# Optimization experiments

Measured on AMD Instinct MI355X. Metric: run time of the kernel, lower is better.

## Reference

```python
import jax, jax.numpy as jnp
import numpy as np

# dims
B, C, H, W = 2, 256, 128, 256
P, G = 9, 8            # num_pts, num_groups
GC = C // G            # group_channels


def setup_inputs() -> dict:
    key = jax.random.key(0)
    ks = jax.random.split(key, 8)
    s = 0.02
    return {
        "feats1": jax.random.normal(ks[0], (B, C, H, W), jnp.float32),
        "feats2": jax.random.normal(ks[1], (B, C, H, W), jnp.float32),
        "anchor_points": jax.random.uniform(ks[2], (B, H * W, 2), jnp.float32),
        "norm1_g": jnp.ones((C,), jnp.float32), "norm1_b": jnp.zeros((C,), jnp.float32),
        "norm2_g": jnp.ones((C,), jnp.float32), "norm2_b": jnp.zeros((C,), jnp.float32),
        "Wv": jax.random.normal(ks[3], (C, C), jnp.float32) * s, "bv": jnp.zeros((C,), jnp.float32),
        "Ww": jax.random.normal(ks[4], (C, G * P), jnp.float32) * s, "bw": jnp.zeros((G * P,), jnp.float32),
        "Wk": jax.random.normal(ks[5], (C, P), jnp.float32) * s, "bk": jnp.zeros((P,), jnp.float32),
        "Wo": jax.random.normal(ks[6], (C, C), jnp.float32) * s, "bo": jnp.zeros((C,), jnp.float32),
    }


def _ln(x, g, b):
    # LayerNorm over the last (channel) axis, eps as torch default
    m = jnp.mean(x, axis=-1, keepdims=True)
    v = jnp.mean(jnp.square(x - m), axis=-1, keepdims=True)
    return (x - m) * jax.lax.rsqrt(v + 1e-5) * g + b


def _bilinear_sample(value, pts):
    # value: (b, H, W, C); pts: (b, N, 2) normalized [0,1] (x, y)
    # grid_sample semantics: align_corners=False, zero padding
    b, h, w, c = value.shape
    x = pts[..., 0] * w - 0.5
    y = pts[..., 1] * h - 0.5
    x0 = jnp.floor(x)
    y0 = jnp.floor(y)
    wx = (x - x0)[..., None]
    wy = (y - y0)[..., None]
    x0i = x0.astype(jnp.int32)
    y0i = y0.astype(jnp.int32)
    vflat = value.reshape(b, h * w, c)

    def gather(yi, xi):
        valid = (yi >= 0) & (yi < h) & (xi >= 0) & (xi < w)
        idx = jnp.clip(yi, 0, h - 1) * w + jnp.clip(xi, 0, w - 1)
        g = jnp.take_along_axis(vflat, idx[..., None], axis=1)
        return g * valid[..., None].astype(value.dtype)

    v00 = gather(y0i, x0i)
    v01 = gather(y0i, x0i + 1)
    v10 = gather(y0i + 1, x0i)
    v11 = gather(y0i + 1, x0i + 1)
    return (v00 * (1 - wx) * (1 - wy) + v01 * wx * (1 - wy)
            + v10 * (1 - wx) * wy + v11 * wx * wy)


def reference(feats1, feats2, anchor_points, norm1_g, norm1_b, norm2_g, norm2_b,
              Wv, bv, Ww, bw, Wk, bk, Wo, bo):
    b, c, h, w = feats1.shape
    hw = h * w
    # to_3d(dim=2): (b, c, h, w) -> (b, hw, c); LayerNorm over c
    x1 = _ln(feats1.reshape(b, c, hw).transpose(0, 2, 1), norm1_g, norm1_b)
    x2 = _ln(feats2.reshape(b, c, hw).transpose(0, 2, 1), norm2_g, norm2_b)

    # value_proj (1x1 conv == per-pixel linear)
    value = (x2 @ Wv + bv).reshape(b, h, w, c)

    # weight_proj -> (b, hw, P, G); channel layout p*G + g; softmax over the P points per group
    logits = (x1 @ Ww + bw).reshape(b, hw, P, G)
    wts = jax.nn.softmax(logits, axis=2)

    # 1D key-point generator: per-pixel learned offsets along x around the anchor
    off = x1 @ Wk + bk                                   # (b, hw, P) normalized offsets
    kx = anchor_points[..., 0:1] + off                   # (b, hw, P)
    ky = jnp.broadcast_to(anchor_points[..., 1:2], kx.shape)
    kp = jnp.stack([kx, ky], axis=-1)                    # (b, hw, P, 2)

    # deformable aggregation: bilinear gather + group-weighted sum over points
    samp = _bilinear_sample(value, kp.reshape(b, hw * P, 2)).reshape(b, hw, P, G, GC)
    agg = jnp.einsum('bnpgc,bnpg->bngc', samp, wts).reshape(b, hw, c)

    out = (agg @ Wo + bo).reshape(b, h, w, c).transpose(0, 3, 1, 2)  # (b, c, h, w)
    return out, kp.reshape(b, h, w, P, 2)
```

## Files before the change

### kernel.cpp

```cpp
#include <hip/hip_runtime.h>
#include <hip/hip_bf16.h>


constexpr int B = 2, C = 256, H = 128, W = 256;
constexpr int HW = H * W;
constexpr int P = 9, G = 8;
constexpr int PIX = 32;
constexpr int NPIX = B * HW;

typedef __attribute__((ext_vector_type(8))) __bf16 bf16x8;
typedef __attribute__((ext_vector_type(4))) float f32x4;

static __device__ __forceinline__ unsigned short f2bf(float x) {
    __hip_bfloat16 h = __float2bfloat16(x);
    return *reinterpret_cast<unsigned short*>(&h);
}
static __device__ __forceinline__ unsigned int pack2(float a, float b) {
    return (unsigned int)f2bf(a) | ((unsigned int)f2bf(b) << 16);
}
static __device__ __forceinline__ bf16x8 ldb8(const unsigned short* p) {
    return *reinterpret_cast<const bf16x8*>(p);
}

__global__ __launch_bounds__(256) void k_prep(
    const float* __restrict__ Ww, const float* __restrict__ Wv,
    const float* __restrict__ Wo,
    unsigned short* __restrict__ WwT, unsigned short* __restrict__ WvT,
    unsigned short* __restrict__ WoT)
{
    int tid = blockIdx.x * 256 + threadIdx.x;
    if (tid < 20480) {
        int n = tid >> 8, k = tid & 255;
        float v = (n < 72) ? Ww[k * 72 + n] : 0.f;
        WwT[tid] = f2bf(v);
    } else if (tid < 20480 + 65536) {
        int i = tid - 20480;
        int n = i >> 8, k = i & 255;
        WvT[i] = f2bf(Wv[k * 256 + n]);
    } else {
        int i = tid - 86016;
        int n = i >> 8, k = i & 255;
        WoT[i] = f2bf(Wo[k * 256 + n]);
    }
}

__global__ __launch_bounds__(256) void k1_ln1(
    const float* __restrict__ feats1,
    const float* __restrict__ anchor,
    const float* __restrict__ g1, const float* __restrict__ b1,
    const float* __restrict__ Wk, const float* __restrict__ bk,
    unsigned short* __restrict__ x1b, float* __restrict__ kp_out)
{
    __shared__ float X[PIX][C + 1];
    __shared__ float red[2][8][PIX];
    __shared__ float meanA[PIX], rstdA[PIX];

    const int t = threadIdx.x;
    const int p = t & 31;
    const int part = t >> 5;
    const int gpix0 = blockIdx.x * PIX;
    const int b = gpix0 >> 15;
    const int n0 = gpix0 & (HW - 1);
    const float* Fb = feats1 + (size_t)b * C * HW;

    #pragma unroll
    for (int i = 0; i < 32; ++i) {
        int c = i * 8 + part;
        X[p][c] = Fb[(size_t)c * HW + n0 + p];
    }
    __syncthreads();

    float s = 0.f, ss = 0.f;
    #pragma unroll
    for (int i = 0; i < 32; ++i) {
        float v = X[p][part * 32 + i];
        s += v; ss += v * v;
    }
    red[0][part][p] = s; red[1][part][p] = ss;
    __syncthreads();
    if (part == 0) {
        float s2 = 0.f, ss2 = 0.f;
        #pragma unroll
        for (int k = 0; k < 8; ++k) { s2 += red[0][k][p]; ss2 += red[1][k][p]; }
        float mean = s2 * (1.f / C);
        float var  = ss2 * (1.f / C) - mean * mean;
        meanA[p] = mean; rstdA[p] = rsqrtf(var + 1e-5f);
    }
    __syncthreads();
    {
        float mean = meanA[p], rstd = rstdA[p];
        #pragma unroll
        for (int i = 0; i < 32; ++i) {
            int c = part * 32 + i;
            X[p][c] = (X[p][c] - mean) * rstd * g1[c] + b1[c];
        }
    }
    __syncthreads();

    {
        unsigned short* row = x1b + ((size_t)gpix0 + p) * C + part * 32;
        #pragma unroll
        for (int i4 = 0; i4 < 8; ++i4) {
            uint2 u;
            u.x = pack2(X[p][part * 32 + i4 * 4 + 0], X[p][part * 32 + i4 * 4 + 1]);
            u.y = pack2(X[p][part * 32 + i4 * 4 + 2], X[p][part * 32 + i4 * 4 + 3]);
            *reinterpret_cast<uint2*>(row + i4 * 4) = u;
        }
    }

    const size_t pixg = (size_t)gpix0 + p;
    const float ax = anchor[pixg * 2 + 0];
    const float ay = anchor[pixg * 2 + 1];
    for (int j = 72 + part; j < 81; j += 8) {
        int pt = j - 72;
        float acc = bk[pt];
        #pragma unroll 4
        for (int c = 0; c < C; ++c) acc += X[p][c] * Wk[c * P + pt];
        size_t o = (pixg * P + pt) * 2;
        kp_out[o] = ax + acc;
        kp_out[o + 1] = ay;
    }
}

__global__ __launch_bounds__(256) void k2_ln2(
    const float* __restrict__ feats2,
    const float* __restrict__ g2, const float* __restrict__ b2,
    unsigned short* __restrict__ x2b)
{
    __shared__ float X[PIX][C + 1];
    __shared__ float red[2][8][PIX];
    __shared__ float meanA[PIX], rstdA[PIX];

    const int t = threadIdx.x;
    const int p = t & 31;
    const int part = t >> 5;
    const int gpix0 = blockIdx.x * PIX;
    const int b = gpix0 >> 15;
    const int n0 = gpix0 & (HW - 1);
    const float* Fb = feats2 + (size_t)b * C * HW;

    #pragma unroll
    for (int i = 0; i < 32; ++i) {
        int c = i * 8 + part;
        X[p][c] = Fb[(size_t)c * HW + n0 + p];
    }
    __syncthreads();

    float s = 0.f, ss = 0.f;
    #pragma unroll
    for (int i = 0; i < 32; ++i) {
        float v = X[p][part * 32 + i];
        s += v; ss += v * v;
    }
    red[0][part][p] = s; red[1][part][p] = ss;
    __syncthreads();
    if (part == 0) {
        float s2 = 0.f, ss2 = 0.f;
        #pragma unroll
        for (int k = 0; k < 8; ++k) { s2 += red[0][k][p]; ss2 += red[1][k][p]; }
        float mean = s2 * (1.f / C);
        float var  = ss2 * (1.f / C) - mean * mean;
        meanA[p] = mean; rstdA[p] = rsqrtf(var + 1e-5f);
    }
    __syncthreads();
    {
        float mean = meanA[p], rstd = rstdA[p];
        unsigned short* row = x2b + ((size_t)gpix0 + p) * C + part * 32;
        #pragma unroll
        for (int i4 = 0; i4 < 8; ++i4) {
            float v0 = (X[p][part * 32 + i4 * 4 + 0] - mean) * rstd * g2[part * 32 + i4 * 4 + 0] + b2[part * 32 + i4 * 4 + 0];
            float v1 = (X[p][part * 32 + i4 * 4 + 1] - mean) * rstd * g2[part * 32 + i4 * 4 + 1] + b2[part * 32 + i4 * 4 + 1];
            float v2 = (X[p][part * 32 + i4 * 4 + 2] - mean) * rstd * g2[part * 32 + i4 * 4 + 2] + b2[part * 32 + i4 * 4 + 2];
            float v3 = (X[p][part * 32 + i4 * 4 + 3] - mean) * rstd * g2[part * 32 + i4 * 4 + 3] + b2[part * 32 + i4 * 4 + 3];
            uint2 u; u.x = pack2(v0, v1); u.y = pack2(v2, v3);
            *reinterpret_cast<uint2*>(row + i4 * 4) = u;
        }
    }
}

__global__ __launch_bounds__(256) void k_gemmw(
    const unsigned short* __restrict__ x1b,
    const unsigned short* __restrict__ WwT,
    const float* __restrict__ bw,
    float* __restrict__ wts)
{
    __shared__ float L[128][81];

    const int t = threadIdx.x;
    const int wave = t >> 6, lane = t & 63;
    const int m_base = blockIdx.x * 128;
    const int m0 = m_base + wave * 32;
    const int l15 = lane & 15, quad = lane >> 4;

    f32x4 acc[2][5];
    #pragma unroll
    for (int ms = 0; ms < 2; ++ms)
        #pragma unroll
        for (int ns = 0; ns < 5; ++ns)
            acc[ms][ns] = (f32x4){0.f, 0.f, 0.f, 0.f};

    size_t aoff[2], boff[5];
    #pragma unroll
    for (int ms = 0; ms < 2; ++ms)
        aoff[ms] = (size_t)(m0 + ms * 16 + l15) * 256 + quad * 8;
    #pragma unroll
    for (int ns = 0; ns < 5; ++ns)
        boff[ns] = (size_t)(ns * 16 + l15) * 256 + quad * 8;

    for (int kk = 0; kk < 8; ++kk) {
        bf16x8 a[2], bfr[5];
        #pragma unroll
        for (int ms = 0; ms < 2; ++ms) a[ms] = ldb8(x1b + aoff[ms] + kk * 32);
        #pragma unroll
        for (int ns = 0; ns < 5; ++ns) bfr[ns] = ldb8(WwT + boff[ns] + kk * 32);
        #pragma unroll
        for (int ms = 0; ms < 2; ++ms)
            #pragma unroll
            for (int ns = 0; ns < 5; ++ns)
                acc[ms][ns] = __builtin_amdgcn_mfma_f32_16x16x32_bf16(a[ms], bfr[ns], acc[ms][ns], 0, 0, 0);
    }

    float bias[5];
    #pragma unroll
    for (int ns = 0; ns < 5; ++ns) {
        int n = ns * 16 + l15;
        bias[ns] = (n < 72) ? bw[n] : 0.f;
    }
    #pragma unroll
    for (int ms = 0; ms < 2; ++ms) {
        #pragma unroll
        for (int ns = 0; ns < 5; ++ns) {
            int n = ns * 16 + l15;
            if (n < 72) {
                #pragma unroll
                for (int r = 0; r < 4; ++r) {
                    int ml = wave * 32 + ms * 16 + quad * 4 + r;
                    L[ml][n] = acc[ms][ns][r] + bias[ns];
                }
            }
        }
    }
    __syncthreads();

    for (int tau = t; tau < 1024; tau += 256) {
        int px = tau >> 3, g = tau & 7;
        float m = -1e30f;
        #pragma unroll
        for (int pt = 0; pt < P; ++pt) m = fmaxf(m, L[px][pt * 8 + g]);
        float e[P], sum = 0.f;
        #pragma unroll
        for (int pt = 0; pt < P; ++pt) { e[pt] = __expf(L[px][pt * 8 + g] - m); sum += e[pt]; }
        float inv = 1.f / sum;
        float* wb = wts + (size_t)(m_base + px) * 72 + g * 9;
        #pragma unroll
        for (int pt = 0; pt < P; ++pt) wb[pt] = e[pt] * inv;
    }
}

__global__ __launch_bounds__(256) void k_gemmv(
    const unsigned short* __restrict__ x2b,
    const unsigned short* __restrict__ WvT,
    const float* __restrict__ bv,
    unsigned short* __restrict__ val)
{
    const int t = threadIdx.x;
    const int wave = t >> 6, lane = t & 63;
    const int m_base = blockIdx.x * 64;
    const int n0 = wave * 64;
    const int l15 = lane & 15, quad = lane >> 4;

    f32x4 acc[4][4];
    #pragma unroll
    for (int ms = 0; ms < 4; ++ms)
        #pragma unroll
        for (int ns = 0; ns < 4; ++ns)
            acc[ms][ns] = (f32x4){0.f, 0.f, 0.f, 0.f};

    size_t aoff[4], boff[4];
    #pragma unroll
    for (int ms = 0; ms < 4; ++ms)
        aoff[ms] = (size_t)(m_base + ms * 16 + l15) * 256 + quad * 8;
    #pragma unroll
    for (int ns = 0; ns < 4; ++ns)
        boff[ns] = (size_t)(n0 + ns * 16 + l15) * 256 + quad * 8;

    for (int kk = 0; kk < 8; ++kk) {
        bf16x8 a[4], bfr[4];
        #pragma unroll
        for (int ms = 0; ms < 4; ++ms) a[ms] = ldb8(x2b + aoff[ms] + kk * 32);
        #pragma unroll
        for (int ns = 0; ns < 4; ++ns) bfr[ns] = ldb8(WvT + boff[ns] + kk * 32);
        #pragma unroll
        for (int ms = 0; ms < 4; ++ms)
            #pragma unroll
            for (int ns = 0; ns < 4; ++ns)
                acc[ms][ns] = __builtin_amdgcn_mfma_f32_16x16x32_bf16(a[ms], bfr[ns], acc[ms][ns], 0, 0, 0);
    }

    float bvr[4];
    #pragma unroll
    for (int ns = 0; ns < 4; ++ns) bvr[ns] = bv[n0 + ns * 16 + l15];

    #pragma unroll
    for (int ms = 0; ms < 4; ++ms) {
        #pragma unroll
        for (int ns = 0; ns < 4; ++ns) {
            int n = n0 + ns * 16 + l15;
            #pragma unroll
            for (int r = 0; r < 4; ++r) {
                int pix = m_base + ms * 16 + quad * 4 + r;
                val[(size_t)pix * 256 + n] = f2bf(acc[ms][ns][r] + bvr[ns]);
            }
        }
    }
}

__global__ __launch_bounds__(256) void k_gather(
    const float* __restrict__ wts,
    const float* __restrict__ kp,
    const unsigned short* __restrict__ val,
    unsigned short* __restrict__ aggb)
{
    __shared__ float Wl[PIX][72];
    __shared__ float KPl[PIX][18];

    const int t = threadIdx.x;
    const int gpix0 = blockIdx.x * PIX;
    const int b = gpix0 >> 15;

    for (int f = t; f < PIX * 72; f += 256)
        ((float*)Wl)[f] = wts[(size_t)gpix0 * 72 + f];
    for (int f = t; f < PIX * 18; f += 256)
        ((float*)KPl)[f] = kp[(size_t)gpix0 * 18 + f];
    __syncthreads();

    const int wave = t >> 6, lane = t & 63;
    const int gl = lane >> 3;
    const unsigned short* vbp = val + (size_t)b * HW * 256 + 4 * lane;

    for (int px = wave; px < PIX; px += 4) {
        const float ay = KPl[px][1];
        float yf = ay * (float)H - 0.5f;
        float y0f = floorf(yf);
        float wy = yf - y0f;
        int y0 = (int)y0f;
        float vy0 = ((unsigned)y0 < (unsigned)H) ? 1.f : 0.f;
        float vy1 = ((unsigned)(y0 + 1) < (unsigned)H) ? 1.f : 0.f;
        int y0c = min(max(y0, 0), H - 1);
        int y1c = min(max(y0 + 1, 0), H - 1);

        float a0 = 0.f, a1 = 0.f, a2 = 0.f, a3 = 0.f;

        #pragma unroll
        for (int pt = 0; pt < P; ++pt) {
            float kx = KPl[px][2 * pt];
            float w  = Wl[px][gl * 9 + pt];
            float xf = kx * (float)W - 0.5f;
            float x0f = floorf(xf);
            float wx = xf - x0f;
            int x0 = (int)x0f;
            float vx0 = ((unsigned)x0 < (unsigned)W) ? 1.f : 0.f;
            float vx1 = ((unsigned)(x0 + 1) < (unsigned)W) ? 1.f : 0.f;
            int x0c = min(max(x0, 0), W - 1);
            int x1c = min(max(x0 + 1, 0), W - 1);

            float c00 = w * (1.f - wx) * (1.f - wy) * vy0 * vx0;
            float c01 = w * wx * (1.f - wy) * vy0 * vx1;
            float c10 = w * (1.f - wx) * wy * vy1 * vx0;
            float c11 = w * wx * wy * vy1 * vx1;

            uint2 u00 = *(const uint2*)(vbp + ((size_t)(y0c * W + x0c) << 8));
            uint2 u01 = *(const uint2*)(vbp + ((size_t)(y0c * W + x1c) << 8));
            uint2 u10 = *(const uint2*)(vbp + ((size_t)(y1c * W + x0c) << 8));
            uint2 u11 = *(const uint2*)(vbp + ((size_t)(y1c * W + x1c) << 8));

            a0 += c00 * __uint_as_float(u00.x << 16) + c01 * __uint_as_float(u01.x << 16)
                + c10 * __uint_as_float(u10.x << 16) + c11 * __uint_as_float(u11.x << 16);
            a1 += c00 * __uint_as_float(u00.x & 0xffff0000u) + c01 * __uint_as_float(u01.x & 0xffff0000u)
                + c10 * __uint_as_float(u10.x & 0xffff0000u) + c11 * __uint_as_float(u11.x & 0xffff0000u);
            a2 += c00 * __uint_as_float(u00.y << 16) + c01 * __uint_as_float(u01.y << 16)
                + c10 * __uint_as_float(u10.y << 16) + c11 * __uint_as_float(u11.y << 16);
            a3 += c00 * __uint_as_float(u00.y & 0xffff0000u) + c01 * __uint_as_float(u01.y & 0xffff0000u)
                + c10 * __uint_as_float(u10.y & 0xffff0000u) + c11 * __uint_as_float(u11.y & 0xffff0000u);
        }

        uint2 o;
        o.x = pack2(a0, a1);
        o.y = pack2(a2, a3);
        *reinterpret_cast<uint2*>(aggb + ((size_t)(gpix0 + px) << 8) + 4 * lane) = o;
    }
}

__global__ __launch_bounds__(256) void k_gemmo(
    const unsigned short* __restrict__ aggb,
    const unsigned short* __restrict__ WoT,
    const float* __restrict__ bo,
    float* __restrict__ out)
{
    const int t = threadIdx.x;
    const int wave = t >> 6, lane = t & 63;
    const int n_base = blockIdx.x * 64;
    const int b = n_base >> 15;
    const int hw0 = n_base & (HW - 1);
    const int m0 = wave * 64;
    const int l15 = lane & 15, quad = lane >> 4;

    f32x4 acc[4][4];
    #pragma unroll
    for (int ms = 0; ms < 4; ++ms)
        #pragma unroll
        for (int ns = 0; ns < 4; ++ns)
            acc[ms][ns] = (f32x4){0.f, 0.f, 0.f, 0.f};

    size_t aoff[4], boff[4];
    #pragma unroll
    for (int ms = 0; ms < 4; ++ms)
        aoff[ms] = (size_t)(m0 + ms * 16 + l15) * 256 + quad * 8;
    #pragma unroll
    for (int ns = 0; ns < 4; ++ns)
        boff[ns] = (size_t)(n_base + ns * 16 + l15) * 256 + quad * 8;

    for (int kk = 0; kk < 8; ++kk) {
        bf16x8 a[4], bfr[4];
        #pragma unroll
        for (int ms = 0; ms < 4; ++ms) a[ms] = ldb8(WoT + aoff[ms] + kk * 32);
        #pragma unroll
        for (int ns = 0; ns < 4; ++ns) bfr[ns] = ldb8(aggb + boff[ns] + kk * 32);
        #pragma unroll
        for (int ms = 0; ms < 4; ++ms)
            #pragma unroll
            for (int ns = 0; ns < 4; ++ns)
                acc[ms][ns] = __builtin_amdgcn_mfma_f32_16x16x32_bf16(a[ms], bfr[ns], acc[ms][ns], 0, 0, 0);
    }

    float bor[4][4];
    #pragma unroll
    for (int ms = 0; ms < 4; ++ms)
        #pragma unroll
        for (int r = 0; r < 4; ++r)
            bor[ms][r] = bo[m0 + ms * 16 + quad * 4 + r];

    #pragma unroll
    for (int ms = 0; ms < 4; ++ms) {
        #pragma unroll
        for (int ns = 0; ns < 4; ++ns) {
            #pragma unroll
            for (int r = 0; r < 4; ++r) {
                int ch = m0 + ms * 16 + quad * 4 + r;
                int pixn = ns * 16 + l15;
                out[((size_t)b * 256 + ch) * HW + hw0 + pixn] = acc[ms][ns][r] + bor[ms][r];
            }
        }
    }
}

extern "C" void kernel_launch(void* const* d_in, const int* in_sizes, int n_in,
                              void* d_out, int out_size, void* d_ws, size_t ws_size,
                              hipStream_t stream)
{
    const float* feats1 = (const float*)d_in[0];
    const float* feats2 = (const float*)d_in[1];
    const float* anchor = (const float*)d_in[2];
    const float* n1g    = (const float*)d_in[3];
    const float* n1b    = (const float*)d_in[4];
    const float* n2g    = (const float*)d_in[5];
    const float* n2b    = (const float*)d_in[6];
    const float* Wv     = (const float*)d_in[7];
    const float* bv     = (const float*)d_in[8];
    const float* Ww     = (const float*)d_in[9];
    const float* bw     = (const float*)d_in[10];
    const float* Wk     = (const float*)d_in[11];
    const float* bk     = (const float*)d_in[12];
    const float* Wo     = (const float*)d_in[13];
    const float* bo     = (const float*)d_in[14];

    float* out = (float*)d_out;
    float* kp  = out + (size_t)B * C * HW;

    unsigned short* R1  = (unsigned short*)d_ws;
    unsigned short* val = (unsigned short*)((char*)d_ws + 33554432);
    float*          wts = (float*)((char*)d_ws + 67108864);
    unsigned short* WwT = (unsigned short*)((char*)d_ws + 85983232);
    unsigned short* WvT = WwT + 20480;
    unsigned short* WoT = WvT + 65536;

    k_prep <<<592,  256, 0, stream>>>(Ww, Wv, Wo, WwT, WvT, WoT);
    k1_ln1 <<<2048, 256, 0, stream>>>(feats1, anchor, n1g, n1b, Wk, bk, R1, kp);
    k_gemmw<<<512,  256, 0, stream>>>(R1, WwT, bw, wts);
    k2_ln2 <<<2048, 256, 0, stream>>>(feats2, n2g, n2b, R1);
    k_gemmv<<<1024, 256, 0, stream>>>(R1, WvT, bv, val);
    k_gather<<<2048,256, 0, stream>>>(wts, kp, val, R1);
    k_gemmo<<<1024, 256, 0, stream>>>(R1, WoT, bo, out);
}
```

Before: 457.4 us.

## Fuse LayerNorms with projection GEMMs and reorder gather by anchor row buckets

```diff
diff --git a/kernel.cpp b/kernel.cpp
--- a/kernel.cpp
+++ b/kernel.cpp
@@ -7,6 +7,7 @@
 constexpr int P = 9, G = 8;
 constexpr int PIX = 32;
 constexpr int NPIX = B * HW;
+constexpr int NBKT = 2 * 129;
 
 typedef __attribute__((ext_vector_type(8))) __bf16 bf16x8;
 typedef __attribute__((ext_vector_type(4))) float f32x4;
@@ -18,7 +19,10 @@
 static __device__ __forceinline__ unsigned int pack2(float a, float b) {
     return (unsigned int)f2bf(a) | ((unsigned int)f2bf(b) << 16);
 }
-static __device__ __forceinline__ bf16x8 ldb8(const unsigned short* p) {
+static __device__ __forceinline__ float bf2f(unsigned short u) {
+    return __uint_as_float((unsigned int)u << 16);
+}
+static __device__ __forceinline__ bf16x8 ldb8g(const unsigned short* p) {
     return *reinterpret_cast<const bf16x8*>(p);
 }
 
@@ -31,8 +35,7 @@
     int tid = blockIdx.x * 256 + threadIdx.x;
     if (tid < 20480) {
         int n = tid >> 8, k = tid & 255;
-        float v = (n < 72) ? Ww[k * 72 + n] : 0.f;
-        WwT[tid] = f2bf(v);
+        WwT[tid] = f2bf((n < 72) ? Ww[k * 72 + n] : 0.f);
     } else if (tid < 20480 + 65536) {
         int i = tid - 20480;
         int n = i >> 8, k = i & 255;
@@ -44,16 +47,57 @@
     }
 }
 
-__global__ __launch_bounds__(256) void k1_ln1(
-    const float* __restrict__ feats1,
-    const float* __restrict__ anchor,
+static __device__ __forceinline__ int bucket_of(const float* anchor, int pix) {
+    float ay = anchor[(size_t)pix * 2 + 1];
+    int y0 = (int)floorf(ay * (float)H - 0.5f);
+    y0 = min(max(y0, -1), H - 1);
+    return (pix >> 15) * 129 + y0 + 1;
+}
+
+__global__ __launch_bounds__(256) void k_hist(
+    const float* __restrict__ anchor, int* __restrict__ hist)
+{
+    int pix = blockIdx.x * 256 + threadIdx.x;
+    atomicAdd(&hist[bucket_of(anchor, pix)], 1);
+}
+
+__global__ __launch_bounds__(256) void k_scan(
+    const int* __restrict__ hist, int* __restrict__ cursor)
+{
+    __shared__ int h[NBKT];
+    int t = threadIdx.x;
+    for (int i = t; i < NBKT; i += 256) h[i] = hist[i];
+    __syncthreads();
+    if (t == 0) {
+        int run = 0;
+        for (int i = 0; i < NBKT; ++i) { int v = h[i]; cursor[i] = run; run += v; }
+    }
+}
+
+__global__ __launch_bounds__(256) void k_scatter(
+    const float* __restrict__ anchor, int* __restrict__ cursor,
+    int* __restrict__ perm)
+{
+    int pix = blockIdx.x * 256 + threadIdx.x;
+    int pos = atomicAdd(&cursor[bucket_of(anchor, pix)], 1);
+    perm[pos] = pix;
+}
+
+__global__ __launch_bounds__(256) void kA(
+    const float* __restrict__ feats1, const float* __restrict__ anchor,
     const float* __restrict__ g1, const float* __restrict__ b1,
     const float* __restrict__ Wk, const float* __restrict__ bk,
-    unsigned short* __restrict__ x1b, float* __restrict__ kp_out)
-{
-    __shared__ float X[PIX][C + 1];
-    __shared__ float red[2][8][PIX];
-    __shared__ float meanA[PIX], rstdA[PIX];
+    const unsigned short* __restrict__ WwT, const float* __restrict__ bw,
+    unsigned short* __restrict__ wtsb, float* __restrict__ kp_out)
+{
+    __shared__ unsigned short Hi[PIX][264];
+    __shared__ __align__(16) char smB[20480];
+    __shared__ float meanA[PIX], rstdA[PIX], axL[PIX], ayL[PIX];
+
+    float* WkL  = (float*)smB;
+    float* red2 = (float*)(smB + 9216);
+    float* red  = (float*)(smB + 18432);
+    float* Lg   = (float*)smB;
 
     const int t = threadIdx.x;
     const int p = t & 31;
@@ -63,71 +107,132 @@
     const int n0 = gpix0 & (HW - 1);
     const float* Fb = feats1 + (size_t)b * C * HW;
 
-    #pragma unroll
-    for (int i = 0; i < 32; ++i) {
-        int c = i * 8 + part;
-        X[p][c] = Fb[(size_t)c * HW + n0 + p];
-    }
-    __syncthreads();
+    for (int i = t; i < 2304; i += 256) WkL[i] = Wk[i];
+    if (t < PIX) {
+        axL[t] = anchor[((size_t)gpix0 + t) * 2 + 0];
+        ayL[t] = anchor[((size_t)gpix0 + t) * 2 + 1];
+    }
+
+    float x[32];
+    #pragma unroll
+    for (int i = 0; i < 32; ++i)
+        x[i] = Fb[(size_t)(part * 32 + i) * HW + n0 + p];
 
     float s = 0.f, ss = 0.f;
     #pragma unroll
-    for (int i = 0; i < 32; ++i) {
-        float v = X[p][part * 32 + i];
-        s += v; ss += v * v;
-    }
-    red[0][part][p] = s; red[1][part][p] = ss;
+    for (int i = 0; i < 32; ++i) { s += x[i]; ss += x[i] * x[i]; }
+    red[part * 32 + p] = s;
+    red[256 + part * 32 + p] = ss;
     __syncthreads();
     if (part == 0) {
         float s2 = 0.f, ss2 = 0.f;
         #pragma unroll
-        for (int k = 0; k < 8; ++k) { s2 += red[0][k][p]; ss2 += red[1][k][p]; }
+        for (int k = 0; k < 8; ++k) { s2 += red[k * 32 + p]; ss2 += red[256 + k * 32 + p]; }
         float mean = s2 * (1.f / C);
         float var  = ss2 * (1.f / C) - mean * mean;
         meanA[p] = mean; rstdA[p] = rsqrtf(var + 1e-5f);
     }
     __syncthreads();
+
     {
         float mean = meanA[p], rstd = rstdA[p];
         #pragma unroll
         for (int i = 0; i < 32; ++i) {
             int c = part * 32 + i;
-            X[p][c] = (X[p][c] - mean) * rstd * g1[c] + b1[c];
-        }
-    }
-    __syncthreads();
+            x[i] = (x[i] - mean) * rstd * g1[c] + b1[c];
+        }
+    }
 
     {
-        unsigned short* row = x1b + ((size_t)gpix0 + p) * C + part * 32;
-        #pragma unroll
-        for (int i4 = 0; i4 < 8; ++i4) {
-            uint2 u;
-            u.x = pack2(X[p][part * 32 + i4 * 4 + 0], X[p][part * 32 + i4 * 4 + 1]);
-            u.y = pack2(X[p][part * 32 + i4 * 4 + 2], X[p][part * 32 + i4 * 4 + 3]);
-            *reinterpret_cast<uint2*>(row + i4 * 4) = u;
-        }
-    }
-
-    const size_t pixg = (size_t)gpix0 + p;
-    const float ax = anchor[pixg * 2 + 0];
-    const float ay = anchor[pixg * 2 + 1];
-    for (int j = 72 + part; j < 81; j += 8) {
-        int pt = j - 72;
-        float acc = bk[pt];
+        float po[9];
+        #pragma unroll
+        for (int pt = 0; pt < 9; ++pt) po[pt] = 0.f;
         #pragma unroll 4
-        for (int c = 0; c < C; ++c) acc += X[p][c] * Wk[c * P + pt];
-        size_t o = (pixg * P + pt) * 2;
-        kp_out[o] = ax + acc;
-        kp_out[o + 1] = ay;
-    }
-}
-
-__global__ __launch_bounds__(256) void k2_ln2(
+        for (int i = 0; i < 32; ++i) {
+            int c = part * 32 + i;
+            float xv = x[i];
+            #pragma unroll
+            for (int pt = 0; pt < 9; ++pt) po[pt] += xv * WkL[c * 9 + pt];
+        }
+        #pragma unroll
+        for (int pt = 0; pt < 9; ++pt) red2[(part * 32 + p) * 9 + pt] = po[pt];
+    }
+
+    {
+        unsigned int* row = (unsigned int*)&Hi[p][part * 32];
+        #pragma unroll
+        for (int i = 0; i < 16; ++i) row[i] = pack2(x[2 * i], x[2 * i + 1]);
+    }
+    __syncthreads();
+
+    for (int tau = t; tau < 288; tau += 256) {
+        int px = tau & 31, pt = tau >> 5;
+        float off = bk[pt];
+        #pragma unroll
+        for (int k = 0; k < 8; ++k) off += red2[(k * 32 + px) * 9 + pt];
+        size_t o = (((size_t)gpix0 + px) * P + pt) * 2;
+        kp_out[o] = axL[px] + off;
+        kp_out[o + 1] = ayL[px];
+    }
+
+    const int wave = t >> 6, lane = t & 63;
+    const int l15 = lane & 15, quad = lane >> 4;
+    const int mt = wave & 1;
+    const int ntb = (wave >> 1) * 3;
+    const int ntc = (wave >> 1) ? 2 : 3;
+
+    f32x4 acc[3];
+    #pragma unroll
+    for (int j = 0; j < 3; ++j) acc[j] = (f32x4){0.f, 0.f, 0.f, 0.f};
+
+    const unsigned short* arow = &Hi[mt * 16 + l15][quad * 8];
+    for (int kk = 0; kk < 8; ++kk) {
+        bf16x8 a = *reinterpret_cast<const bf16x8*>(arow + kk * 32);
+        for (int j = 0; j < 3; ++j) {
+            if (j < ntc) {
+                bf16x8 bfr = ldb8g(WwT + (size_t)((ntb + j) * 16 + l15) * 256 + quad * 8 + kk * 32);
+                acc[j] = __builtin_amdgcn_mfma_f32_16x16x32_bf16(a, bfr, acc[j], 0, 0, 0);
+            }
+        }
+    }
+    __syncthreads();
+
+    #pragma unroll
+    for (int j = 0; j < 3; ++j) {
+        if (j < ntc) {
+            int n = (ntb + j) * 16 + l15;
+            if (n < 72) {
+                float bwn = bw[n];
+                #pragma unroll
+                for (int r = 0; r < 4; ++r)
+                    Lg[(mt * 16 + quad * 4 + r) * 81 + n] = acc[j][r] + bwn;
+            }
+        }
+    }
+    __syncthreads();
+
+    {
+        int px = t >> 3, g = t & 7;
+        float m = -1e30f;
+        #pragma unroll
+        for (int pt = 0; pt < P; ++pt) m = fmaxf(m, Lg[px * 81 + pt * 8 + g]);
+        float e[P], sum = 0.f;
+        #pragma unroll
+        for (int pt = 0; pt < P; ++pt) { e[pt] = __expf(Lg[px * 81 + pt * 8 + g] - m); sum += e[pt]; }
+        float inv = 1.f / sum;
+        unsigned short* wb = wtsb + ((size_t)gpix0 + px) * 72 + g * 9;
+        #pragma unroll
+        for (int pt = 0; pt < P; ++pt) wb[pt] = f2bf(e[pt] * inv);
+    }
+}
+
+__global__ __launch_bounds__(256) void kB(
     const float* __restrict__ feats2,
     const float* __restrict__ g2, const float* __restrict__ b2,
-    unsigned short* __restrict__ x2b)
-{
-    __shared__ float X[PIX][C + 1];
+    const unsigned short* __restrict__ WvT, const float* __restrict__ bv,
+    unsigned short* __restrict__ val)
+{
+    __shared__ unsigned short Hi[PIX][264];
     __shared__ float red[2][8][PIX];
     __shared__ float meanA[PIX], rstdA[PIX];
 
@@ -139,19 +244,14 @@
     const int n0 = gpix0 & (HW - 1);
     const float* Fb = feats2 + (size_t)b * C * HW;
 
-    #pragma unroll
-    for (int i = 0; i < 32; ++i) {
-        int c = i * 8 + part;
-        X[p][c] = Fb[(size_t)c * HW + n0 + p];
-    }
-    __syncthreads();
+    float x[32];
+    #pragma unroll
+    for (int i = 0; i < 32; ++i)
+        x[i] = Fb[(size_t)(part * 32 + i) * HW + n0 + p];
 
     float s = 0.f, ss = 0.f;
     #pragma unroll
-    for (int i = 0; i < 32; ++i) {
-        float v = X[p][part * 32 + i];
-        s += v; ss += v * v;
-    }
+    for (int i = 0; i < 32; ++i) { s += x[i]; ss += x[i] * x[i]; }
     red[0][part][p] = s; red[1][part][p] = ss;
     __syncthreads();
     if (part == 0) {
@@ -165,180 +265,92 @@
     __syncthreads();
     {
         float mean = meanA[p], rstd = rstdA[p];
-        unsigned short* row = x2b + ((size_t)gpix0 + p) * C + part * 32;
-        #pragma unroll
-        for (int i4 = 0; i4 < 8; ++i4) {
-            float v0 = (X[p][part * 32 + i4 * 4 + 0] - mean) * rstd * g2[part * 32 + i4 * 4 + 0] + b2[part * 32 + i4 * 4 + 0];
-            float v1 = (X[p][part * 32 + i4 * 4 + 1] - mean) * rstd * g2[part * 32 + i4 * 4 + 1] + b2[part * 32 + i4 * 4 + 1];
-            float v2 = (X[p][part * 32 + i4 * 4 + 2] - mean) * rstd * g2[part * 32 + i4 * 4 + 2] + b2[part * 32 + i4 * 4 + 2];
-            float v3 = (X[p][part * 32 + i4 * 4 + 3] - mean) * rstd * g2[part * 32 + i4 * 4 + 3] + b2[part * 32 + i4 * 4 + 3];
-            uint2 u; u.x = pack2(v0, v1); u.y = pack2(v2, v3);
-            *reinterpret_cast<uint2*>(row + i4 * 4) = u;
-        }
-    }
-}
-
-__global__ __launch_bounds__(256) void k_gemmw(
-    const unsigned short* __restrict__ x1b,
-    const unsigned short* __restrict__ WwT,
-    const float* __restrict__ bw,
-    float* __restrict__ wts)
-{
-    __shared__ float L[128][81];
-
-    const int t = threadIdx.x;
+        unsigned int* row = (unsigned int*)&Hi[p][part * 32];
+        #pragma unroll
+        for (int i = 0; i < 16; ++i) {
+            float v0 = (x[2 * i] - mean) * rstd * g2[part * 32 + 2 * i] + b2[part * 32 + 2 * i];
+            float v1 = (x[2 * i + 1] - mean) * rstd * g2[part * 32 + 2 * i + 1] + b2[part * 32 + 2 * i + 1];
+            row[i] = pack2(v0, v1);
+        }
+    }
+    __syncthreads();
+
     const int wave = t >> 6, lane = t & 63;
-    const int m_base = blockIdx.x * 128;
-    const int m0 = m_base + wave * 32;
     const int l15 = lane & 15, quad = lane >> 4;
-
-    f32x4 acc[2][5];
-    #pragma unroll
-    for (int ms = 0; ms < 2; ++ms)
-        #pragma unroll
-        for (int ns = 0; ns < 5; ++ns)
-            acc[ms][ns] = (f32x4){0.f, 0.f, 0.f, 0.f};
-
-    size_t aoff[2], boff[5];
-    #pragma unroll
-    for (int ms = 0; ms < 2; ++ms)
-        aoff[ms] = (size_t)(m0 + ms * 16 + l15) * 256 + quad * 8;
-    #pragma unroll
-    for (int ns = 0; ns < 5; ++ns)
-        boff[ns] = (size_t)(ns * 16 + l15) * 256 + quad * 8;
+    const int m0 = wave * 64;
+
+    f32x4 acc[4][2];
+    #pragma unroll
+    for (int ms = 0; ms < 4; ++ms)
+        #pragma unroll
+        for (int nt = 0; nt < 2; ++nt)
+            acc[ms][nt] = (f32x4){0.f, 0.f, 0.f, 0.f};
 
     for (int kk = 0; kk < 8; ++kk) {
-        bf16x8 a[2], bfr[5];
-        #pragma unroll
-        for (int ms = 0; ms < 2; ++ms) a[ms] = ldb8(x1b + aoff[ms] + kk * 32);
-        #pragma unroll
-        for (int ns = 0; ns < 5; ++ns) bfr[ns] = ldb8(WwT + boff[ns] + kk * 32);
-        #pragma unroll
-        for (int ms = 0; ms < 2; ++ms)
-            #pragma unroll
-            for (int ns = 0; ns < 5; ++ns)
-                acc[ms][ns] = __builtin_amdgcn_mfma_f32_16x16x32_bf16(a[ms], bfr[ns], acc[ms][ns], 0, 0, 0);
-    }
-
-    float bias[5];
-    #pragma unroll
-    for (int ns = 0; ns < 5; ++ns) {
-        int n = ns * 16 + l15;
-        bias[ns] = (n < 72) ? bw[n] : 0.f;
-    }
-    #pragma unroll
-    for (int ms = 0; ms < 2; ++ms) {
-        #pragma unroll
-        for (int ns = 0; ns < 5; ++ns) {
-            int n = ns * 16 + l15;
-            if (n < 72) {
-                #pragma unroll
-                for (int r = 0; r < 4; ++r) {
-                    int ml = wave * 32 + ms * 16 + quad * 4 + r;
-                    L[ml][n] = acc[ms][ns][r] + bias[ns];
-                }
-            }
-        }
-    }
-    __syncthreads();
-
-    for (int tau = t; tau < 1024; tau += 256) {
-        int px = tau >> 3, g = tau & 7;
-        float m = -1e30f;
-        #pragma unroll
-        for (int pt = 0; pt < P; ++pt) m = fmaxf(m, L[px][pt * 8 + g]);
-        float e[P], sum = 0.f;
-        #pragma unroll
-        for (int pt = 0; pt < P; ++pt) { e[pt] = __expf(L[px][pt * 8 + g] - m); sum += e[pt]; }
-        float inv = 1.f / sum;
-        float* wb = wts + (size_t)(m_base + px) * 72 + g * 9;
-        #pragma unroll
-        for (int pt = 0; pt < P; ++pt) wb[pt] = e[pt] * inv;
-    }
-}
-
-__global__ __launch_bounds__(256) void k_gemmv(
-    const unsigned short* __restrict__ x2b,
-    const unsigned short* __restrict__ WvT,
-    const float* __restrict__ bv,
-    unsigned short* __restrict__ val)
-{
-    const int t = threadIdx.x;
-    const int wave = t >> 6, lane = t & 63;
-    const int m_base = blockIdx.x * 64;
-    const int n0 = wave * 64;
-    const int l15 = lane & 15, quad = lane >> 4;
-
-    f32x4 acc[4][4];
-    #pragma unroll
-    for (int ms = 0; ms < 4; ++ms)
-        #pragma unroll
-        for (int ns = 0; ns < 4; ++ns)
-            acc[ms][ns] = (f32x4){0.f, 0.f, 0.f, 0.f};
-
-    size_t aoff[4], boff[4];
-    #pragma unroll
-    for (int ms = 0; ms < 4; ++ms)
-        aoff[ms] = (size_t)(m_base + ms * 16 + l15) * 256 + quad * 8;
-    #pragma unroll
-    for (int ns = 0; ns < 4; ++ns)
-        boff[ns] = (size_t)(n0 + ns * 16 + l15) * 256 + quad * 8;
-
-    for (int kk = 0; kk < 8; ++kk) {
-        bf16x8 a[4], bfr[4];
-        #pragma unroll
-        for (int ms = 0; ms < 4; ++ms) a[ms] = ldb8(x2b + aoff[ms] + kk * 32);
-        #pragma unroll
-        for (int ns = 0; ns < 4; ++ns) bfr[ns] = ldb8(WvT + boff[ns] + kk * 32);
+        bf16x8 a[4], bfr[2];
+        #pragma unroll
+        for (int ms = 0; ms < 4; ++ms)
+            a[ms] = ldb8g(WvT + (size_t)(m0 + ms * 16 + l15) * 256 + quad * 8 + kk * 32);
+        #pragma unroll
+        for (int nt = 0; nt < 2; ++nt)
+            bfr[nt] = *reinterpret_cast<const bf16x8*>(&Hi[nt * 16 + l15][quad * 8 + kk * 32]);
         #pragma unroll
         for (int ms = 0; ms < 4; ++ms)
             #pragma unroll
-            for (int ns = 0; ns < 4; ++ns)
-                acc[ms][ns] = __builtin_amdgcn_mfma_f32_16x16x32_bf16(a[ms], bfr[ns], acc[ms][ns], 0, 0, 0);
-    }
-
-    float bvr[4];
-    #pragma unroll
-    for (int ns = 0; ns < 4; ++ns) bvr[ns] = bv[n0 + ns * 16 + l15];
+            for (int nt = 0; nt < 2; ++nt)
+                acc[ms][nt] = __builtin_amdgcn_mfma_f32_16x16x32_bf16(a[ms], bfr[nt], acc[ms][nt], 0, 0, 0);
+    }
 
     #pragma unroll
     for (int ms = 0; ms < 4; ++ms) {
-        #pragma unroll
-        for (int ns = 0; ns < 4; ++ns) {
-            int n = n0 + ns * 16 + l15;
-            #pragma unroll
-            for (int r = 0; r < 4; ++r) {
-                int pix = m_base + ms * 16 + quad * 4 + r;
-                val[(size_t)pix * 256 + n] = f2bf(acc[ms][ns][r] + bvr[ns]);
-            }
+        int ch0 = m0 + ms * 16 + quad * 4;
+        float b0 = bv[ch0], b1v = bv[ch0 + 1], b2v = bv[ch0 + 2], b3 = bv[ch0 + 3];
+        #pragma unroll
+        for (int nt = 0; nt < 2; ++nt) {
+            int pix = gpix0 + nt * 16 + l15;
+            uint2 o;
+            o.x = pack2(acc[ms][nt][0] + b0, acc[ms][nt][1] + b1v);
+            o.y = pack2(acc[ms][nt][2] + b2v, acc[ms][nt][3] + b3);
+            *reinterpret_cast<uint2*>(val + (size_t)pix * 256 + ch0) = o;
         }
     }
 }
 
 __global__ __launch_bounds__(256) void k_gather(
-    const float* __restrict__ wts,
+    const unsigned short* __restrict__ wtsb,
     const float* __restrict__ kp,
     const unsigned short* __restrict__ val,
+    const int* __restrict__ perm,
     unsigned short* __restrict__ aggb)
 {
     __shared__ float Wl[PIX][72];
     __shared__ float KPl[PIX][18];
+    __shared__ int pixL[PIX];
 
     const int t = threadIdx.x;
     const int gpix0 = blockIdx.x * PIX;
-    const int b = gpix0 >> 15;
-
-    for (int f = t; f < PIX * 72; f += 256)
-        ((float*)Wl)[f] = wts[(size_t)gpix0 * 72 + f];
-    for (int f = t; f < PIX * 18; f += 256)
-        ((float*)KPl)[f] = kp[(size_t)gpix0 * 18 + f];
+
+    if (t < PIX) pixL[t] = perm[gpix0 + t];
+    __syncthreads();
+
+    {
+        int px = t >> 3, j = t & 7;
+        int pix = pixL[px];
+        const unsigned short* wrow = wtsb + (size_t)pix * 72 + j * 9;
+        #pragma unroll
+        for (int k = 0; k < 9; ++k) Wl[px][j * 9 + k] = bf2f(wrow[k]);
+        const float* krow = kp + (size_t)pix * 18;
+        for (int k = j; k < 18; k += 8) KPl[px][k] = krow[k];
+    }
     __syncthreads();
 
     const int wave = t >> 6, lane = t & 63;
     const int gl = lane >> 3;
-    const unsigned short* vbp = val + (size_t)b * HW * 256 + 4 * lane;
 
     for (int px = wave; px < PIX; px += 4) {
+        const int pix = pixL[px];
+        const unsigned short* vbp = val + ((size_t)(pix >> 15) * HW) * 256 + 4 * lane;
+
         const float ay = KPl[px][1];
         float yf = ay * (float)H - 0.5f;
         float y0f = floorf(yf);
@@ -387,7 +399,7 @@
         uint2 o;
         o.x = pack2(a0, a1);
         o.y = pack2(a2, a3);
-        *reinterpret_cast<uint2*>(aggb + ((size_t)(gpix0 + px) << 8) + 4 * lane) = o;
+        *reinterpret_cast<uint2*>(aggb + ((size_t)pix << 8) + 4 * lane) = o;
     }
 }
 
@@ -423,9 +435,9 @@
     for (int kk = 0; kk < 8; ++kk) {
         bf16x8 a[4], bfr[4];
         #pragma unroll
-        for (int ms = 0; ms < 4; ++ms) a[ms] = ldb8(WoT + aoff[ms] + kk * 32);
-        #pragma unroll
-        for (int ns = 0; ns < 4; ++ns) bfr[ns] = ldb8(aggb + boff[ns] + kk * 32);
+        for (int ms = 0; ms < 4; ++ms) a[ms] = ldb8g(WoT + aoff[ms] + kk * 32);
+        #pragma unroll
+        for (int ns = 0; ns < 4; ++ns) bfr[ns] = ldb8g(aggb + boff[ns] + kk * 32);
         #pragma unroll
         for (int ms = 0; ms < 4; ++ms)
             #pragma unroll
@@ -447,8 +459,7 @@
             #pragma unroll
             for (int r = 0; r < 4; ++r) {
                 int ch = m0 + ms * 16 + quad * 4 + r;
-                int pixn = ns * 16 + l15;
-                out[((size_t)b * 256 + ch) * HW + hw0 + pixn] = acc[ms][ns][r] + bor[ms][r];
+                out[((size_t)b * 256 + ch) * HW + hw0 + ns * 16 + l15] = acc[ms][ns][r] + bor[ms][r];
             }
         }
     }
@@ -477,18 +488,24 @@
     float* out = (float*)d_out;
     float* kp  = out + (size_t)B * C * HW;
 
-    unsigned short* R1  = (unsigned short*)d_ws;
-    unsigned short* val = (unsigned short*)((char*)d_ws + 33554432);
-    float*          wts = (float*)((char*)d_ws + 67108864);
-    unsigned short* WwT = (unsigned short*)((char*)d_ws + 85983232);
-    unsigned short* WvT = WwT + 20480;
-    unsigned short* WoT = WvT + 65536;
-
-    k_prep <<<592,  256, 0, stream>>>(Ww, Wv, Wo, WwT, WvT, WoT);
-    k1_ln1 <<<2048, 256, 0, stream>>>(feats1, anchor, n1g, n1b, Wk, bk, R1, kp);
-    k_gemmw<<<512,  256, 0, stream>>>(R1, WwT, bw, wts);
-    k2_ln2 <<<2048, 256, 0, stream>>>(feats2, n2g, n2b, R1);
-    k_gemmv<<<1024, 256, 0, stream>>>(R1, WvT, bv, val);
-    k_gather<<<2048,256, 0, stream>>>(wts, kp, val, R1);
-    k_gemmo<<<1024, 256, 0, stream>>>(R1, WoT, bo, out);
-}
+    char* ws = (char*)d_ws;
+    unsigned short* val  = (unsigned short*)(ws);
+    unsigned short* aggb = (unsigned short*)(ws + 33554432);
+    unsigned short* wtsb = (unsigned short*)(ws + 67108864);
+    unsigned short* WwT  = (unsigned short*)(ws + 76546048);
+    unsigned short* WvT  = (unsigned short*)(ws + 76587008);
+    unsigned short* WoT  = (unsigned short*)(ws + 76718080);
+    int* perm   = (int*)(ws + 76849152);
+    int* hist   = (int*)(ws + 77111296);
+    int* cursor = hist + NBKT;
+
+    hipMemsetAsync(hist, 0, NBKT * sizeof(int), stream);
+    k_prep   <<<592,  256, 0, stream>>>(Ww, Wv, Wo, WwT, WvT, WoT);
+    k_hist   <<<256,  256, 0, stream>>>(anchor, hist);
+    k_scan   <<<1,    256, 0, stream>>>(hist, cursor);
+    k_scatter<<<256,  256, 0, stream>>>(anchor, cursor, perm);
+    kA       <<<2048, 256, 0, stream>>>(feats1, anchor, n1g, n1b, Wk, bk, WwT, bw, wtsb, kp);
+    kB       <<<2048, 256, 0, stream>>>(feats2, n2g, n2b, WvT, bv, val);
+    k_gather <<<2048, 256, 0, stream>>>(wtsb, kp, val, perm, aggb);
+    k_gemmo  <<<1024, 256, 0, stream>>>(aggb, WoT, bo, out);
+}
```

Result: slower. 479.6 us (+4.9%).
